# Kernel optimization log

Measured on AMD Instinct MI355X. Metric: run time of the kernel, lower is better.

Reference implementation:

```python
import jax, jax.numpy as jnp
import numpy as np

N_NODES = 100000
N_GRAPHS = 512


def gcn_conv(x, W, b, src, dst, n_nodes):
    """PyG GCNConv: out = D^{-1/2} (A + I) D^{-1/2} (x W) + b, scatter at dst."""
    xw = x @ W  # [N, out_dim]
    # add self loops
    loop = jnp.arange(n_nodes, dtype=src.dtype)
    src_f = jnp.concatenate([src, loop])
    dst_f = jnp.concatenate([dst, loop])
    # symmetric normalization: deg from unit edge weights on dst
    deg = jax.ops.segment_sum(jnp.ones_like(dst_f, dtype=xw.dtype), dst_f,
                              num_segments=n_nodes)
    dinv = jnp.where(deg > 0, jax.lax.rsqrt(deg), 0.0)
    norm = dinv[src_f] * dinv[dst_f]  # [E+N]
    msg = xw[src_f] * norm[:, None]   # gather + scale, [E+N, out_dim]
    out = jax.ops.segment_sum(msg, dst_f, num_segments=n_nodes)
    return out + b


def global_mean_pool(x, batch, num_graphs):
    s = jax.ops.segment_sum(x, batch, num_segments=num_graphs)
    cnt = jax.ops.segment_sum(jnp.ones((x.shape[0],), x.dtype), batch,
                              num_segments=num_graphs)
    return s / jnp.maximum(cnt, 1.0)[:, None]


def setup_inputs() -> dict:
    key = jax.random.key(0)
    ks = jax.random.split(key, 10)
    d_in, h1, h2, d_out = 128, 128, 128, 32
    n_edges = 1600000
    x = jax.random.normal(ks[0], (N_NODES, d_in), dtype=jnp.float32)
    edge_index = jax.random.randint(ks[1], (2, n_edges), 0, N_NODES, dtype=jnp.int64)
    batch = jnp.sort(jax.random.randint(ks[2], (N_NODES,), 0, N_GRAPHS, dtype=jnp.int64))
    s1 = 1.0 / np.sqrt(d_in)
    s2 = 1.0 / np.sqrt(h1)
    s3 = 1.0 / np.sqrt(h2)
    W1 = jax.random.uniform(ks[3], (d_in, h1), jnp.float32, -s1, s1)
    b1 = jnp.zeros((h1,), jnp.float32)
    W2 = jax.random.uniform(ks[4], (h1, h2), jnp.float32, -s2, s2)
    b2 = jnp.zeros((h2,), jnp.float32)
    Wl = jax.random.uniform(ks[5], (h2, d_out), jnp.float32, -s3 * np.sqrt(6.0), s3 * np.sqrt(6.0))
    bl = jax.random.uniform(ks[6], (d_out,), jnp.float32, -s3, s3)
    return {"x": x, "edge_index": edge_index, "batch": batch,
            "W1": W1, "b1": b1, "W2": W2, "b2": b2, "Wl": Wl, "bl": bl}


def reference(x, edge_index, batch, W1, b1, W2, b2, Wl, bl):
    src, dst = edge_index[0], edge_index[1]
    h = gcn_conv(x, W1, b1, src, dst, N_NODES)
    h = jax.nn.relu(h)
    h = gcn_conv(h, W2, b2, src, dst, N_NODES)
    g = global_mean_pool(h, batch, N_GRAPHS)
    g = jax.nn.relu(g)
    return g @ Wl + bl
```

## Files before the change

kernel.cpp:

```cpp
#include <hip/hip_runtime.h>
#include <hip/hip_fp16.h>

#define DIM 128
#define NGRAPH 512
#define BUCKET_SHIFT 9
#define BUCKET_NODES 512

typedef _Float16 half8 __attribute__((ext_vector_type(8)));
typedef float floatx4 __attribute__((ext_vector_type(4)));

__device__ __forceinline__ int detect64(const int* __restrict__ ei) {
  int all0 = 1;
#pragma unroll
  for (int k = 0; k < 32; ++k) all0 &= (ei[2 * k + 1] == 0);
  return all0;
}

__device__ __forceinline__ int edge_at(const int* p, long long idx, int is64) {
  return is64 ? p[idx * 2] : p[(size_t)idx];
}

__global__ __launch_bounds__(256) void k_bucket_hist(const int* __restrict__ ei, int E,
                                                     int* __restrict__ bucket_count,
                                                     int nbuck) {
  __shared__ int h[256];
  int tid = threadIdx.x;
  h[tid] = 0;
  __syncthreads();
  int is64 = detect64(ei);
  int half = E >> 1;
  if (is64) {
    const int4* dp = (const int4*)(ei + 2 * (size_t)E);
    for (int t = blockIdx.x * 256 + tid; t < half; t += gridDim.x * 256) {
      int4 d = dp[t];
      atomicAdd(&h[d.x >> BUCKET_SHIFT], 1);
      atomicAdd(&h[d.z >> BUCKET_SHIFT], 1);
    }
  } else {
    const int2* dp = (const int2*)(ei + (size_t)E);
    for (int t = blockIdx.x * 256 + tid; t < half; t += gridDim.x * 256) {
      int2 d = dp[t];
      atomicAdd(&h[d.x >> BUCKET_SHIFT], 1);
      atomicAdd(&h[d.y >> BUCKET_SHIFT], 1);
    }
  }
  __syncthreads();
  if (tid < nbuck && h[tid]) atomicAdd(&bucket_count[tid], h[tid]);
  if ((E & 1) && blockIdx.x == 0 && tid == 0) {
    int d = edge_at(ei, (long long)E + (E - 1), is64);
    atomicAdd(&bucket_count[d >> BUCKET_SHIFT], 1);
  }
}

__global__ __launch_bounds__(256) void k_bucket_scan(const int* __restrict__ bucket_count,
                                                     int* __restrict__ bucket_off,
                                                     int* __restrict__ bucket_cursor,
                                                     int* __restrict__ row_off,
                                                     int nbuck, int N, int E) {
  __shared__ int s[256];
  int t = threadIdx.x;
  int v = (t < nbuck) ? bucket_count[t] : 0;
  s[t] = v;
  __syncthreads();
  for (int off = 1; off < 256; off <<= 1) {
    int u = (t >= off) ? s[t - off] : 0;
    __syncthreads();
    s[t] += u;
    __syncthreads();
  }
  int excl = s[t] - v;
  if (t < nbuck) { bucket_off[t] = excl; bucket_cursor[t] = excl; }
  if (t == 0) { bucket_off[nbuck] = E; row_off[N] = E; }
}

__global__ __launch_bounds__(256) void k_scatter(const int* __restrict__ ei, int E,
                                                 int* __restrict__ flag,
                                                 int* __restrict__ bucket_cursor,
                                                 int2* __restrict__ staging, int nbuck) {
  __shared__ int h[256];
  __shared__ int basebuf[256];
  int tid = threadIdx.x;
  int half = E >> 1;
  int ppb = (half + gridDim.x - 1) / gridDim.x;
  int lo = blockIdx.x * ppb;
  int hi = min(lo + ppb, half);
  h[tid] = 0;
  __syncthreads();
  int is64 = detect64(ei);
  if (blockIdx.x == 0 && tid == 0) *flag = is64;
  if (is64) {
    const int4* dp = (const int4*)(ei + 2 * (size_t)E);
    for (int t = lo + tid; t < hi; t += 256) {
      int4 d = dp[t];
      atomicAdd(&h[d.x >> BUCKET_SHIFT], 1);
      atomicAdd(&h[d.z >> BUCKET_SHIFT], 1);
    }
  } else {
    const int2* dp = (const int2*)(ei + (size_t)E);
    for (int t = lo + tid; t < hi; t += 256) {
      int2 d = dp[t];
      atomicAdd(&h[d.x >> BUCKET_SHIFT], 1);
      atomicAdd(&h[d.y >> BUCKET_SHIFT], 1);
    }
  }
  __syncthreads();
  if (tid < nbuck) {
    int c = h[tid];
    if (c) basebuf[tid] = atomicAdd(&bucket_cursor[tid], c);
    h[tid] = 0;
  }
  __syncthreads();
  if (is64) {
    const int4* sp = (const int4*)ei;
    const int4* dp = (const int4*)(ei + 2 * (size_t)E);
    for (int t = lo + tid; t < hi; t += 256) {
      int4 sv = sp[t];
      int4 dv = dp[t];
      int b0 = dv.x >> BUCKET_SHIFT;
      int l0 = atomicAdd(&h[b0], 1);
      staging[basebuf[b0] + l0] = make_int2(sv.x, dv.x);
      int b1 = dv.z >> BUCKET_SHIFT;
      int l1 = atomicAdd(&h[b1], 1);
      staging[basebuf[b1] + l1] = make_int2(sv.z, dv.z);
    }
  } else {
    const int2* sp = (const int2*)ei;
    const int2* dp = (const int2*)(ei + (size_t)E);
    for (int t = lo + tid; t < hi; t += 256) {
      int2 sv = sp[t];
      int2 dv = dp[t];
      int b0 = dv.x >> BUCKET_SHIFT;
      int l0 = atomicAdd(&h[b0], 1);
      staging[basebuf[b0] + l0] = make_int2(sv.x, dv.x);
      int b1 = dv.y >> BUCKET_SHIFT;
      int l1 = atomicAdd(&h[b1], 1);
      staging[basebuf[b1] + l1] = make_int2(sv.y, dv.y);
    }
  }
  if ((E & 1) && blockIdx.x == 0 && tid == 0) {
    int s0 = edge_at(ei, E - 1, is64);
    int d0 = edge_at(ei, (long long)E + (E - 1), is64);
    int pos = atomicAdd(&bucket_cursor[d0 >> BUCKET_SHIFT], 1);
    staging[pos] = make_int2(s0, d0);
  }
}

__global__ __launch_bounds__(256) void k_csr_build(const int2* __restrict__ staging,
                                                   const int* __restrict__ bucket_off,
                                                   int* __restrict__ row_off,
                                                   float* __restrict__ dinv,
                                                   int* __restrict__ csr_src, int N) {
  __shared__ int cnt_s[BUCKET_NODES];
  __shared__ int s[256];
  int tid = threadIdx.x;
  int b = blockIdx.x;
  int base = b << BUCKET_SHIFT;
  cnt_s[tid] = 0;
  cnt_s[tid + 256] = 0;
  __syncthreads();
  int start = bucket_off[b], end = bucket_off[b + 1];
  for (int i = start + tid; i < end; i += 256) {
    int2 e = staging[i];
    atomicAdd(&cnt_s[e.y - base], 1);
  }
  __syncthreads();
  int a0 = cnt_s[2 * tid], a1 = cnt_s[2 * tid + 1];
  int ps = a0 + a1;
  s[tid] = ps;
  __syncthreads();
  for (int off = 1; off < 256; off <<= 1) {
    int u = (tid >= off) ? s[tid - off] : 0;
    __syncthreads();
    s[tid] += u;
    __syncthreads();
  }
  int excl = s[tid] - ps;
  int r0 = start + excl;
  int r1 = r0 + a0;
  cnt_s[2 * tid] = r0;
  cnt_s[2 * tid + 1] = r1;
  int n0 = base + 2 * tid, n1 = n0 + 1;
  if (n0 < N) { row_off[n0] = r0; dinv[n0] = rsqrtf((float)(a0 + 1)); }
  if (n1 < N) { row_off[n1] = r1; dinv[n1] = rsqrtf((float)(a1 + 1)); }
  __syncthreads();
  for (int i = start + tid; i < end; i += 256) {
    int2 e = staging[i];
    int pos = atomicAdd(&cnt_s[e.y - base], 1);
    csr_src[pos] = e.x;
  }
}

__global__ __launch_bounds__(256) void k_gemm_mfma(
    const float* __restrict__ A, const float* __restrict__ W,
    const float* __restrict__ dinv, __half* __restrict__ Y, int M) {
  __shared__ _Float16 WH[16384];
  __shared__ _Float16 WL[16384];
  __shared__ _Float16 OT[4][16 * 128];
  int tid = threadIdx.x;

  for (int idx = tid; idx < 2048; idx += 256) {
    int l = idx & 63, c = (idx >> 6) & 7, s = idx >> 9;
    int kbase = s * 32 + ((l >> 4) << 3);
    int col = c * 16 + (l & 15);
#pragma unroll
    for (int j = 0; j < 8; ++j) {
      float w = W[(kbase + j) * 128 + col];
      _Float16 hh = (_Float16)w;
      WH[idx * 8 + j] = hh;
      WL[idx * 8 + j] = (_Float16)(w - (float)hh);
    }
  }
  __syncthreads();

  int wid = tid >> 6, l = tid & 63;
  int row0 = blockIdx.x * 64 + wid * 16;
  int arow = row0 + (l & 15);
  if (arow >= M) arow = M - 1;

  floatx4 acc[8];
#pragma unroll
  for (int c = 0; c < 8; ++c) acc[c] = (floatx4){0.f, 0.f, 0.f, 0.f};

#pragma unroll
  for (int s = 0; s < 4; ++s) {
    const float* ap = &A[(size_t)arow * 128 + s * 32 + ((l >> 4) << 3)];
    float4 f0 = *(const float4*)ap;
    float4 f1 = *(const float4*)(ap + 4);
    float fv[8] = {f0.x, f0.y, f0.z, f0.w, f1.x, f1.y, f1.z, f1.w};
    half8 ah, alo;
#pragma unroll
    for (int j = 0; j < 8; ++j) {
      _Float16 hh = (_Float16)fv[j];
      ah[j] = hh;
      alo[j] = (_Float16)(fv[j] - (float)hh);
    }
#pragma unroll
    for (int c = 0; c < 8; ++c) {
      int fi = ((s * 8 + c) * 64 + l) * 8;
      half8 bh = *(half8*)&WH[fi];
      half8 bl8 = *(half8*)&WL[fi];
      acc[c] = __builtin_amdgcn_mfma_f32_16x16x32_f16(ah, bh, acc[c], 0, 0, 0);
      acc[c] = __builtin_amdgcn_mfma_f32_16x16x32_f16(alo, bh, acc[c], 0, 0, 0);
      acc[c] = __builtin_amdgcn_mfma_f32_16x16x32_f16(ah, bl8, acc[c], 0, 0, 0);
    }
  }

  _Float16* ot = &OT[wid][0];
  int lrb = (l >> 4) * 4;
  float dv[4];
#pragma unroll
  for (int r = 0; r < 4; ++r) {
    int gr = row0 + lrb + r;
    dv[r] = (gr < M) ? dinv[gr] : 0.f;
  }
#pragma unroll
  for (int c = 0; c < 8; ++c)
#pragma unroll
    for (int r = 0; r < 4; ++r)
      ot[(lrb + r) * 128 + c * 16 + (l & 15)] = (_Float16)(acc[c][r] * dv[r]);
  const float4* otf = (const float4*)ot;
#pragma unroll
  for (int q = 0; q < 4; ++q) {
    int idx = q * 64 + l;
    int lrow = idx >> 4;
    int coff = (idx & 15) * 8;
    int grow = row0 + lrow;
    if (grow < M) *(float4*)&Y[(size_t)grow * 128 + coff] = otf[idx];
  }
}

__global__ __launch_bounds__(256) void k_aggregate(
    const __half* __restrict__ y, const int* __restrict__ csr_src,
    const int* __restrict__ row_off, const float* __restrict__ dinv,
    const float* __restrict__ bias, float* __restrict__ out, int do_relu, int N) {
  __shared__ int sidx[1024];
  int tid = threadIdx.x;
  int n0 = blockIdx.x * 4;
  int lastn = min(n0 + 4, N);
  int blockBeg = row_off[n0];
  int blockEnd = row_off[lastn];
  int len = blockEnd - blockBeg;
  int nload = min(len, 1024);
  for (int t = tid; t < nload; t += 256) sidx[t] = csr_src[blockBeg + t];
  __syncthreads();
  int node = n0 + (tid >> 6);
  if (node >= N) return;
  int lane = tid & 63;
  int beg = row_off[node], end = row_off[node + 1];
  float di = dinv[node];
  const __half2* base = (const __half2*)y;
  __half2 sv = base[(size_t)node * 64 + lane];
  float ax = __low2float(sv), ay = __high2float(sv);
  int e = beg;
  if (len <= nload) {
    for (; e + 8 <= end; e += 8) {
      int idx[8];
#pragma unroll
      for (int j = 0; j < 8; ++j) idx[j] = sidx[e - blockBeg + j];
      __half2 v[8];
#pragma unroll
      for (int j = 0; j < 8; ++j) v[j] = base[(size_t)idx[j] * 64 + lane];
#pragma unroll
      for (int j = 0; j < 8; ++j) { ax += __low2float(v[j]); ay += __high2float(v[j]); }
    }
    for (; e < end; ++e) {
      __half2 v0 = base[(size_t)sidx[e - blockBeg] * 64 + lane];
      ax += __low2float(v0); ay += __high2float(v0);
    }
  } else {
    for (; e < end; ++e) {
      __half2 v0 = base[(size_t)csr_src[e] * 64 + lane];
      ax += __low2float(v0); ay += __high2float(v0);
    }
  }
  float2 b = ((const float2*)bias)[lane];
  ax = di * ax + b.x;
  ay = di * ay + b.y;
  if (do_relu) { ax = fmaxf(ax, 0.f); ay = fmaxf(ay, 0.f); }
  float2 o; o.x = ax; o.y = ay;
  ((float2*)out)[(size_t)node * 64 + lane] = o;
}

__global__ __launch_bounds__(128) void k_pool_final(
    const float* __restrict__ h, const int* __restrict__ batch,
    const float* __restrict__ Wl, const float* __restrict__ bl,
    float* __restrict__ out, int n, const int* __restrict__ flag) {
  __shared__ float sW[128 * 32];
  __shared__ float sg[128];
  __shared__ int bounds[2];
  int tid = threadIdx.x;
  int gid = blockIdx.x;
  for (int t = tid; t < 128 * 32; t += 128) sW[t] = Wl[t];
  int is64 = *flag;
  if (tid < 2) {
    int target = gid + tid;
    int lo = 0, hi = n;
    while (lo < hi) {
      int mid = (lo + hi) >> 1;
      int bv = is64 ? batch[2 * mid] : batch[mid];
      if (bv < target) lo = mid + 1; else hi = mid;
    }
    bounds[tid] = lo;
  }
  __syncthreads();
  int lo = bounds[0], hi = bounds[1];
  float s = 0.f;
  for (int r = lo; r < hi; ++r) s += h[(size_t)r * 128 + tid];
  sg[tid] = fmaxf(s / fmaxf((float)(hi - lo), 1.f), 0.f);
  __syncthreads();
  if (tid < 32) {
    float acc = bl[tid];
#pragma unroll 8
    for (int k = 0; k < 128; ++k) acc += sg[k] * sW[k * 32 + tid];
    out[gid * 32 + tid] = acc;
  }
}

extern "C" void kernel_launch(void* const* d_in, const int* in_sizes, int n_in,
                              void* d_out, int out_size, void* d_ws, size_t ws_size,
                              hipStream_t stream) {
  const float* x   = (const float*)d_in[0];
  const int* ei    = (const int*)d_in[1];
  const int* batch = (const int*)d_in[2];
  const float* W1  = (const float*)d_in[3];
  const float* b1  = (const float*)d_in[4];
  const float* W2  = (const float*)d_in[5];
  const float* b2  = (const float*)d_in[6];
  const float* Wl  = (const float*)d_in[7];
  const float* bl  = (const float*)d_in[8];
  float* out = (float*)d_out;

  const int N = in_sizes[0] / DIM;
  const int E = in_sizes[1] / 2;
  const int NBUCK = (N + BUCKET_NODES - 1) >> BUCKET_SHIFT;

  size_t need = (size_t)N * DIM * 2 + (size_t)N * DIM * 4 + (size_t)E * 4
              + (size_t)(N + 1) * 4 + (size_t)N * 4 + 3 * 1088 + 64;
  if (ws_size < need) return;

  char* w = (char*)d_ws;
  __half* bufY  = (__half*)w; w += (size_t)N * DIM * 2;
  float* bufH   = (float*)w;  w += (size_t)N * DIM * 4;
  int* csr_src  = (int*)w;    w += (size_t)E * 4;
  int* row_off  = (int*)w;    w += (size_t)(N + 1) * 4;
  float* dinv   = (float*)w;  w += (size_t)N * 4;
  int* bucket_count  = (int*)w; w += 1088;
  int* bucket_off    = (int*)w; w += 1088;
  int* bucket_cursor = (int*)w; w += 1088;
  int* flag     = (int*)w;    w += 64;
  int2* staging = (int2*)bufY;

  hipMemsetAsync(bucket_count, 0, 1088, stream);
  k_bucket_hist<<<1024, 256, 0, stream>>>(ei, E, bucket_count, NBUCK);
  k_bucket_scan<<<1, 256, 0, stream>>>(bucket_count, bucket_off, bucket_cursor,
                                       row_off, NBUCK, N, E);
  k_scatter<<<1024, 256, 0, stream>>>(ei, E, flag, bucket_cursor, staging, NBUCK);
  k_csr_build<<<NBUCK, 256, 0, stream>>>(staging, bucket_off, row_off, dinv, csr_src, N);

  k_gemm_mfma<<<(N + 63) / 64, 256, 0, stream>>>(x, W1, dinv, bufY, N);
  k_aggregate<<<(N + 3) / 4, 256, 0, stream>>>(bufY, csr_src, row_off, dinv, b1, bufH, 1, N);
  k_gemm_mfma<<<(N + 63) / 64, 256, 0, stream>>>(bufH, W2, dinv, bufY, N);
  k_aggregate<<<(N + 3) / 4, 256, 0, stream>>>(bufY, csr_src, row_off, dinv, b2, bufH, 0, N);
  k_pool_final<<<NGRAPH, 128, 0, stream>>>(bufH, batch, Wl, bl, out, N, flag);
}
```

Before: 459.2 us.

## Split mean pooling into node-parallel partial sums with atomics plus final linear kernel

Replaces the one-block-per-graph pooling kernel with a kernel where each block sums 128 consecutive nodes, flushes a run-length partial sum per graph segment via atomicAdd, and then runs a separate small kernel for the mean, ReLU and final linear layer. This spreads the pooling reads over about 782 blocks instead of 512 blocks with serial row loops of about 195 rows each, which should improve bandwidth use. In exchange it adds atomics, an extra memset and an extra launch, and the float sums now depend on atomic ordering.

```diff
diff --git a/kernel.cpp b/kernel.cpp
--- a/kernel.cpp
+++ b/kernel.cpp
@@ -321,39 +321,55 @@
   ((float2*)out)[(size_t)node * 64 + lane] = o;
 }
 
-__global__ __launch_bounds__(128) void k_pool_final(
+__global__ __launch_bounds__(128) void k_pool_partial(
     const float* __restrict__ h, const int* __restrict__ batch,
+    float* __restrict__ pooled, int* __restrict__ pcnt, int n,
+    const int* __restrict__ flag) {
+  __shared__ int sbatch[128];
+  int tid = threadIdx.x;
+  int n0 = blockIdx.x * 128;
+  int n1 = min(n0 + 128, n);
+  int cnt = n1 - n0;
+  int is64 = *flag;
+  if (tid < cnt) sbatch[tid] = is64 ? batch[2 * (n0 + tid)] : batch[n0 + tid];
+  __syncthreads();
+  float acc = 0.f;
+  int gcur = sbatch[0];
+  int runlen = 0;
+  for (int r = 0; r < cnt; ++r) {
+    int g = sbatch[r];
+    if (g != gcur) {
+      atomicAdd(&pooled[(size_t)gcur * 128 + tid], acc);
+      if (tid == 0) atomicAdd(&pcnt[gcur], runlen);
+      acc = 0.f; runlen = 0; gcur = g;
+    }
+    acc += h[(size_t)(n0 + r) * 128 + tid];
+    ++runlen;
+  }
+  atomicAdd(&pooled[(size_t)gcur * 128 + tid], acc);
+  if (tid == 0) atomicAdd(&pcnt[gcur], runlen);
+}
+
+__global__ __launch_bounds__(256) void k_final2(
+    const float* __restrict__ pooled, const int* __restrict__ pcnt,
     const float* __restrict__ Wl, const float* __restrict__ bl,
-    float* __restrict__ out, int n, const int* __restrict__ flag) {
+    float* __restrict__ out) {
   __shared__ float sW[128 * 32];
-  __shared__ float sg[128];
-  __shared__ int bounds[2];
-  int tid = threadIdx.x;
-  int gid = blockIdx.x;
-  for (int t = tid; t < 128 * 32; t += 128) sW[t] = Wl[t];
-  int is64 = *flag;
-  if (tid < 2) {
-    int target = gid + tid;
-    int lo = 0, hi = n;
-    while (lo < hi) {
-      int mid = (lo + hi) >> 1;
-      int bv = is64 ? batch[2 * mid] : batch[mid];
-      if (bv < target) lo = mid + 1; else hi = mid;
-    }
-    bounds[tid] = lo;
-  }
-  __syncthreads();
-  int lo = bounds[0], hi = bounds[1];
-  float s = 0.f;
-  for (int r = lo; r < hi; ++r) s += h[(size_t)r * 128 + tid];
-  sg[tid] = fmaxf(s / fmaxf((float)(hi - lo), 1.f), 0.f);
-  __syncthreads();
-  if (tid < 32) {
-    float acc = bl[tid];
+  __shared__ float sg[8][128];
+  int tid = threadIdx.x;
+  for (int t = tid; t < 128 * 32; t += 256) sW[t] = Wl[t];
+  int r = blockIdx.x * 8 + (tid >> 5);
+  int c = tid & 31;
+  float inv = 1.f / fmaxf((float)pcnt[r], 1.f);
+#pragma unroll
+  for (int q = 0; q < 4; ++q)
+    sg[tid >> 5][c * 4 + q] = fmaxf(pooled[(size_t)r * 128 + c * 4 + q] * inv, 0.f);
+  __syncthreads();
+  const float* g = sg[tid >> 5];
+  float acc = bl[c];
 #pragma unroll 8
-    for (int k = 0; k < 128; ++k) acc += sg[k] * sW[k * 32 + tid];
-    out[gid * 32 + tid] = acc;
-  }
+  for (int k = 0; k < 128; ++k) acc += g[k] * sW[k * 32 + c];
+  out[r * 32 + c] = acc;
 }
 
 extern "C" void kernel_launch(void* const* d_in, const int* in_sizes, int n_in,
@@ -375,7 +391,8 @@
   const int NBUCK = (N + BUCKET_NODES - 1) >> BUCKET_SHIFT;
 
   size_t need = (size_t)N * DIM * 2 + (size_t)N * DIM * 4 + (size_t)E * 4
-              + (size_t)(N + 1) * 4 + (size_t)N * 4 + 3 * 1088 + 64;
+              + (size_t)(N + 1) * 4 + (size_t)N * 4 + 3 * 1088 + 64
+              + (size_t)NGRAPH * DIM * 4 + NGRAPH * 4;
   if (ws_size < need) return;
 
   char* w = (char*)d_ws;
@@ -388,9 +405,12 @@
   int* bucket_off    = (int*)w; w += 1088;
   int* bucket_cursor = (int*)w; w += 1088;
   int* flag     = (int*)w;    w += 64;
+  float* pooled = (float*)w;  w += (size_t)NGRAPH * DIM * 4;
+  int* pcnt     = (int*)w;    w += NGRAPH * 4;
   int2* staging = (int2*)bufY;
 
   hipMemsetAsync(bucket_count, 0, 1088, stream);
+  hipMemsetAsync(pooled, 0, (size_t)NGRAPH * DIM * 4 + NGRAPH * 4, stream);
   k_bucket_hist<<<1024, 256, 0, stream>>>(ei, E, bucket_count, NBUCK);
   k_bucket_scan<<<1, 256, 0, stream>>>(bucket_count, bucket_off, bucket_cursor,
                                        row_off, NBUCK, N, E);
@@ -401,5 +421,6 @@
   k_aggregate<<<(N + 3) / 4, 256, 0, stream>>>(bufY, csr_src, row_off, dinv, b1, bufH, 1, N);
   k_gemm_mfma<<<(N + 63) / 64, 256, 0, stream>>>(bufH, W2, dinv, bufY, N);
   k_aggregate<<<(N + 3) / 4, 256, 0, stream>>>(bufY, csr_src, row_off, dinv, b2, bufH, 0, N);
-  k_pool_final<<<NGRAPH, 128, 0, stream>>>(bufH, batch, Wl, bl, out, N, flag);
-}
+  k_pool_partial<<<(N + 127) / 128, 128, 0, stream>>>(bufH, batch, pooled, pcnt, N, flag);
+  k_final2<<<NGRAPH / 8, 256, 0, stream>>>(pooled, pcnt, Wl, bl, out);
+}
```

Measured after the change: 441.1 us. 1.04x faster.
